# Kernel optimization log

Measured on AMD Instinct MI355X. Metric: run time of the kernel, lower is better.

Reference implementation:

```python
import jax, jax.numpy as jnp
import numpy as np

N = 100000      # nodes
E = 800000      # edges
IN1 = 128       # gcn input feature dim
IN2 = 64        # lstm input feature dim
H = 128         # hidden_channels
B = 32          # lstm batch
T = 200         # lstm seq len
OUT = 1         # out_channels
TARGET = jnp.array([0, 1000, 2000, 3000, 4000, 5000, 6000, 7000])  # numgcnE=8


def setup_inputs() -> dict:
    key = jax.random.key(0)
    ks = jax.random.split(key, 20)
    s = 0.05
    inp = {
        "data0": jax.random.normal(ks[0], (B, T, IN2), jnp.float32),
        "data1": jax.random.normal(ks[1], (N, IN1), jnp.float32),
        "edge_index": jax.random.randint(ks[2], (2, E), 0, N, dtype=jnp.int64),
        # GCNConv layers (weight stored [in, out])
        "W1": jax.random.normal(ks[3], (IN1, H), jnp.float32) * s,
        "b1": jnp.zeros((H,), jnp.float32),
        "W2": jax.random.normal(ks[4], (H, H), jnp.float32) * s,
        "b2": jnp.zeros((H,), jnp.float32),
        # LSTM1 (gate order i,f,g,o as in torch)
        "Wih1": jax.random.normal(ks[5], (4 * H, IN2), jnp.float32) * s,
        "Whh1": jax.random.normal(ks[6], (4 * H, H), jnp.float32) * s,
        "bih1": jnp.zeros((4 * H,), jnp.float32),
        "bhh1": jnp.zeros((4 * H,), jnp.float32),
        # LSTM2
        "Wih2": jax.random.normal(ks[7], (4 * H, H), jnp.float32) * s,
        "Whh2": jax.random.normal(ks[8], (4 * H, H), jnp.float32) * s,
        "bih2": jnp.zeros((4 * H,), jnp.float32),
        "bhh2": jnp.zeros((4 * H,), jnp.float32),
        # MLP head: (numgcnE+1)*H -> (numgcnE+1)*H/2 -> OUT
        "m1_w": jax.random.normal(ks[9], (9 * H, 9 * H // 2), jnp.float32) * s,
        "m1_b": jnp.zeros((9 * H // 2,), jnp.float32),
        "m2_w": jax.random.normal(ks[10], (9 * H // 2, OUT), jnp.float32) * s,
        "m2_b": jnp.zeros((OUT,), jnp.float32),
    }
    return inp


def gcn_conv(x, W, b, src, dst, n):
    # PyG GCNConv: self-loops + symmetric normalization, then scatter-add.
    xw = x @ W                                                     # [N, H]
    ones = jnp.ones(src.shape[0], xw.dtype)
    deg = jax.ops.segment_sum(ones, dst, num_segments=n) + 1.0     # +1 self-loop
    dinv = jax.lax.rsqrt(deg)                                      # [N]
    norm = dinv[src] * dinv[dst]                                   # [E]
    agg = jax.ops.segment_sum(xw[src] * norm[:, None], dst, num_segments=n)
    agg = agg + xw * (dinv * dinv)[:, None]                        # self-loop msgs
    return agg + b


def lstm_final(x_tbi, Wih, Whh, bih, bhh):
    # x_tbi: [T, Bsz, in]; returns final hidden state h_T [Bsz, H]
    Bsz = x_tbi.shape[1]
    Hh = Whh.shape[1]
    bias = bih + bhh

    def step(carry, xt):
        h, c = carry
        g = xt @ Wih.T + h @ Whh.T + bias                          # [Bsz, 4H]
        i, f, gg, o = jnp.split(g, 4, axis=-1)
        c = jax.nn.sigmoid(f) * c + jax.nn.sigmoid(i) * jnp.tanh(gg)
        h = jax.nn.sigmoid(o) * jnp.tanh(c)
        return (h, c), None

    init = (jnp.zeros((Bsz, Hh), x_tbi.dtype), jnp.zeros((Bsz, Hh), x_tbi.dtype))
    (h, c), _ = jax.lax.scan(step, init, x_tbi)
    return h


def reference(data0, data1, edge_index, W1, b1, W2, b2,
              Wih1, Whh1, bih1, bhh1, Wih2, Whh2, bih2, bhh2,
              m1_w, m1_b, m2_w, m2_b):
    src, dst = edge_index[0], edge_index[1]
    n = data1.shape[0]
    # two GCN layers with ReLU
    h = jax.nn.relu(gcn_conv(data1, W1, b1, src, dst, n))
    h = jax.nn.relu(gcn_conv(h, W2, b2, src, dst, n))
    g = h[TARGET].reshape(-1)                                      # [numgcnE*H]
    # lstm1 over [B, T, IN2] (batch_first) -> final h_n [B, H]
    h1 = lstm_final(jnp.swapaxes(data0, 0, 1), Wih1, Whh1, bih1, bhh1)
    # lstm2 consumes h_n[None] as [batch=1, seq=B, H] -> final h [1, H]
    h2 = lstm_final(h1[:, None, :], Wih2, Whh2, bih2, bhh2)[0]     # [H]
    d = jnp.concatenate([g, h2])                                   # [(numgcnE+1)*H]
    return (d @ m1_w + m1_b) @ m2_w + m2_b                         # [OUT]
```

## Files before the change

### kernel.cpp

```cpp
#include <hip/hip_runtime.h>
#include <hip/hip_bf16.h>
#include <cstring>

using bf16 = __hip_bfloat16;
typedef _Float16 h2v __attribute__((ext_vector_type(2)));
typedef _Float16 h8v __attribute__((ext_vector_type(8)));

#if __has_builtin(__builtin_amdgcn_fdot2)
__device__ __forceinline__ float FDOT2(h2v a, h2v b, float c) {
    return __builtin_amdgcn_fdot2(a, b, c, false);
}
#else
__device__ __forceinline__ float FDOT2(h2v a, h2v b, float c) {
    return c + (float)a.x * (float)b.x + (float)a.y * (float)b.y;
}
#endif

__device__ __forceinline__ float sigm_f(float x) {
    return __builtin_amdgcn_rcpf(1.f + __expf(-x));
}
__device__ __forceinline__ float tanh_f(float x) {
    return 1.f - 2.f * __builtin_amdgcn_rcpf(1.f + __expf(2.f * x));
}

__device__ __forceinline__ float xor32_get(float x) {
#if __has_builtin(__builtin_amdgcn_permlane32_swap)
    typedef unsigned uv2 __attribute__((ext_vector_type(2)));
    union { float f; unsigned u; } cv; cv.f = x;
    uv2 r = __builtin_amdgcn_permlane32_swap(cv.u, cv.u, false, false);
    union { unsigned u; float f; } rv; rv.u = r[1];
    return rv.f;
#else
    return __shfl_xor(x, 32);
#endif
}

constexpr int NH    = 128;
constexpr int G4    = 512;
constexpr int TSEQ  = 200;
constexpr int BBATCH= 32;
constexpr int NTGT  = 8;

constexpr int LCAP1 = 1024;
constexpr int S1CAP = LCAP1 + NTGT;
constexpr int LCAP2 = 8192;
constexpr int S2CAP = LCAP2 + S1CAP;

constexpr size_t algn(size_t x) { return (x + 255) & ~size_t(255); }
constexpr size_t OFF_GX1  = 0;
constexpr size_t OFF_GX2  = algn(OFF_GX1  + 6400ull * G4 * 4);
constexpr size_t OFF_DEG  = algn(OFF_GX2  + 32ull * G4 * 4);
constexpr size_t OFF_DINV = algn(OFF_DEG  + 100000ull * 4);
constexpr size_t OFF_SL1  = algn(OFF_DINV + 100000ull * 4);
constexpr size_t OFF_SL2  = algn(OFF_SL1  + 100000ull * 4);
constexpr size_t OFF_CNT  = algn(OFF_SL2  + 100000ull * 4);
constexpr size_t OFF_L1   = algn(OFF_CNT  + 64);
constexpr size_t OFF_S1   = algn(OFF_L1   + (size_t)LCAP1 * 8);
constexpr size_t OFF_L2   = algn(OFF_S1   + (size_t)S1CAP * 4);
constexpr size_t OFF_S2   = algn(OFF_L2   + (size_t)LCAP2 * 8);
constexpr size_t OFF_XW1  = algn(OFF_S2   + (size_t)S2CAP * 4);
constexpr size_t OFF_H1   = algn(OFF_XW1  + (size_t)S2CAP * NH * 4);
constexpr size_t OFF_XW2  = algn(OFF_H1   + (size_t)S1CAP * NH * 4);
constexpr size_t OFF_DVEC = algn(OFF_XW2  + (size_t)S1CAP * NH * 4);
constexpr size_t OFF_H1F  = algn(OFF_DVEC + 1152ull * 4);
constexpr size_t OFF_CACC = algn(OFF_H1F  + 32ull * NH * 4);
constexpr size_t WS_NEEDED = OFF_CACC + 576ull * 4;

__device__ __forceinline__ int edge_at(const int* ei, int E, int is64, int row, int e) {
    return is64 ? ei[(((size_t)row * E) + e) * 2] : ei[((size_t)row * E) + e];
}

__device__ __forceinline__ float dinv_of(const int* deg, int v) {
    return rsqrtf((float)deg[v] + 1.0f);
}

__global__ void k_init(const int* ei, int* deg, int* slot1, int* slot2, int* cnt,
                       float* h1, int n, unsigned int* out, unsigned int canary) {
    int i0 = blockIdx.x * 256 + threadIdx.x;
    int gstride = gridDim.x * 256;
    if (i0 < 14) cnt[i0] = 0;
    if (i0 == 15) cnt[15] = (ei[1] == 0 && ei[3] == 0 && ei[5] == 0 && ei[7] == 0) ? 1 : 0;
    if (i0 == 16) out[0] = canary;
    for (int i = i0; i < S1CAP * NH; i += gstride) h1[i] = 0.f;
    for (int i = i0; i < n; i += gstride) { deg[i] = 0; slot1[i] = -1; slot2[i] = -1; }
}

__global__ void k_deg_l1(const int* ei, int E, int* deg, int2* l1, int* cnt) {
    int is64 = cnt[15];
    for (int e = blockIdx.x * 256 + threadIdx.x; e < E; e += gridDim.x * 256) {
        int d = edge_at(ei, E, is64, 1, e);
        if ((unsigned)d < 100000u) atomicAdd(&deg[d], 1);
        if (d <= 7000 && d >= 0 && d % 1000 == 0) {
            int s = edge_at(ei, E, is64, 0, e);
            int idx = atomicAdd(&cnt[0], 1);
            if (idx < LCAP1) l1[idx] = make_int2(s, d);
        }
    }
}

__global__ void k_s1(const int2* l1, int* cnt, int* slot1, int* s1list,
                     int* slot2, int* s2list) {
    __shared__ int ns1;
    if (threadIdx.x == 0) ns1 = 0;
    __syncthreads();
    int m = min(cnt[0], LCAP1);
    for (int i = threadIdx.x; i < NTGT + m; i += blockDim.x) {
        int v = (i < NTGT) ? i * 1000 : l1[i - NTGT].x;
        if ((unsigned)v >= 100000u) continue;
        int old = atomicCAS(&slot1[v], -1, -2);
        if (old == -1) {
            int idx = atomicAdd(&ns1, 1);
            if (idx < S1CAP) { s1list[idx] = v; atomicExch(&slot1[v], idx); }
        }
    }
    __syncthreads();
    int n1 = min(ns1, S1CAP);
    if (threadIdx.x == 0) cnt[1] = n1;
    for (int i = threadIdx.x; i < n1; i += blockDim.x) {
        int v = s1list[i];
        int old = atomicCAS(&slot2[v], -1, -2);
        if (old == -1) {
            int idx = atomicAdd(&cnt[2], 1);
            if (idx < S2CAP) { s2list[idx] = v; atomicExch(&slot2[v], idx); }
        }
    }
}

__global__ void k_l2(const int* ei, int E, const int* slot1,
                     int2* l2, int* cnt, int* slot2, int* s2list) {
    int is64 = cnt[15];
    for (int e = blockIdx.x * 256 + threadIdx.x; e < E; e += gridDim.x * 256) {
        int d = edge_at(ei, E, is64, 1, e);
        if ((unsigned)d >= 100000u) continue;
        if (slot1[d] >= 0) {
            int s = edge_at(ei, E, is64, 0, e);
            if ((unsigned)s >= 100000u) continue;
            int idx = atomicAdd(&cnt[3], 1);
            if (idx < LCAP2) l2[idx] = make_int2(s, d);
            int old = atomicCAS(&slot2[s], -1, -2);
            if (old == -1) {
                int j = atomicAdd(&cnt[2], 1);
                if (j < S2CAP) { s2list[j] = s; atomicExch(&slot2[s], j); }
            }
        }
    }
}


__global__ void k_xw1(const float* x, const float* W, const int* s2list, const int* cnt, float* xw1) {
    int i = blockIdx.x;
    if (i >= min(cnt[2], S2CAP)) return;
    int node = s2list[i];
    __shared__ float xs[NH];
    int c = threadIdx.x;
    xs[c] = x[(size_t)node * NH + c];
    __syncthreads();
    float acc = 0.f;
    #pragma unroll 8
    for (int k = 0; k < NH; k++) acc += xs[k] * W[(size_t)k * NH + c];
    xw1[(size_t)i * NH + c] = acc;
}

__global__ void k_h1scat(const float* xw1, const int2* l2, const int* cnt,
                         const int* slot1, const int* slot2, const int* deg, float* h1) {
    int e = blockIdx.x;
    if (e >= min(cnt[3], LCAP2)) return;
    int2 sd = l2[e];
    int t1 = slot1[sd.y], s2 = slot2[sd.x];
    if (t1 < 0 || t1 >= S1CAP || s2 < 0 || s2 >= S2CAP) return;
    float w = dinv_of(deg, sd.x) * dinv_of(deg, sd.y);
    atomicAdd(&h1[t1 * NH + threadIdx.x],
              xw1[(size_t)s2 * NH + threadIdx.x] * w);
}

__global__ void k_xw2(const float* h1, const float* xw1, const float* W, const float* b1,
                      const int* cnt, const int* s1list, const int* slot2, const int* deg,
                      float* xw2) {
    int i = blockIdx.x;
    if (i >= min(cnt[1], S1CAP)) return;
    __shared__ float xs[NH];
    int c = threadIdx.x;
    int node = s1list[i];
    int s2i = slot2[node];
    if (s2i < 0 || s2i >= S2CAP) s2i = 0;
    float v = dinv_of(deg, node);
    xs[c] = fmaxf(h1[i * NH + c] + xw1[(size_t)s2i * NH + c] * (v * v) + b1[c], 0.f);
    __syncthreads();
    float acc = 0.f;
    #pragma unroll 8
    for (int k = 0; k < NH; k++) acc += xs[k] * W[(size_t)k * NH + c];
    xw2[(size_t)i * NH + c] = acc;
}

__global__ void k_gout(const float* xw2, const int2* l1, const int* cnt,
                       const int* slot1, const int* deg, const float* b2, float* dvec) {
    int t = blockIdx.x;
    int tgt = t * 1000;
    int c = threadIdx.x;
    float vt = dinv_of(deg, tgt);
    int st = slot1[tgt]; if (st < 0 || st >= S1CAP) st = 0;
    float acc = xw2[(size_t)st * NH + c] * vt * vt;
    int m = min(cnt[0], LCAP1);
    for (int e = 0; e < m; e++) {
        int2 sd = l1[e];
        if (sd.y == tgt) {
            int ss = slot1[sd.x];
            if (ss >= 0 && ss < S1CAP)
                acc += xw2[(size_t)ss * NH + c] * dinv_of(deg, sd.x) * vt;
        }
    }
    acc += b2[c];
    dvec[t * NH + c] = fmaxf(acc, 0.f);
}


__global__ __launch_bounds__(256) void k_gx1hw(const float* data0, const float* Wih,
                                               const float* bih, const float* bhh, float* gx,
                                               const float* m1w, const float* m1b,
                                               const float* m2w, const float* m2b, float* hw) {
    int tid = threadIdx.x;
    if (blockIdx.x >= 800) {
        int hb = blockIdx.x - 800;
        int wv = tid >> 6, ln = tid & 63;
        if (hb < 18) {
            #pragma unroll 4
            for (int rr = 0; rr < 16; rr++) {
                int row = hb * 64 + wv * 16 + rr;
                float s = 0.f;
                #pragma unroll
                for (int j = ln; j < 576; j += 64) s += m1w[(size_t)row * 576 + j] * m2w[j];
                #pragma unroll
                for (int off = 32; off > 0; off >>= 1) s += __shfl_down(s, off, 64);
                if (ln == 0) hw[row] = s;
            }
        } else if (wv == 0) {
            float s = 0.f;
            for (int j = ln; j < 576; j += 64) s += m1b[j] * m2w[j];
            #pragma unroll
            for (int off = 32; off > 0; off >>= 1) s += __shfl_down(s, off, 64);
            if (ln == 0) hw[1152] = s + m2b[0];
        }
        return;
    }
    constexpr int LDP = 68;
    __shared__ float As[64 * LDP];
    __shared__ float Bs[64 * LDP];
    int rb = blockIdx.x >> 3;
    int gb = blockIdx.x & 7;
    int r0 = rb * 64, g0 = gb * 64;
    for (int i = tid; i < 64 * 64; i += 256) {
        int rr = i >> 6, k = i & 63;
        int r = r0 + rr, b = r & 31, t = r >> 5;
        As[rr * LDP + k] = data0[((size_t)b * TSEQ + t) * 64 + k];
        Bs[rr * LDP + k] = Wih[(size_t)(g0 + rr) * 64 + k];
    }
    __syncthreads();
    int tr = (tid & 15) * 4;
    int tg = (tid >> 4) * 4;
    float acc[4][4] = {};
    #pragma unroll
    for (int k4 = 0; k4 < 16; k4++) {
        float4 a0 = *(const float4*)&As[(tr + 0) * LDP + k4 * 4];
        float4 a1 = *(const float4*)&As[(tr + 1) * LDP + k4 * 4];
        float4 a2 = *(const float4*)&As[(tr + 2) * LDP + k4 * 4];
        float4 a3 = *(const float4*)&As[(tr + 3) * LDP + k4 * 4];
        float4 b0 = *(const float4*)&Bs[(tg + 0) * LDP + k4 * 4];
        float4 b1 = *(const float4*)&Bs[(tg + 1) * LDP + k4 * 4];
        float4 b2 = *(const float4*)&Bs[(tg + 2) * LDP + k4 * 4];
        float4 b3 = *(const float4*)&Bs[(tg + 3) * LDP + k4 * 4];
        const float4 av[4] = {a0, a1, a2, a3};
        const float4 bv[4] = {b0, b1, b2, b3};
        #pragma unroll
        for (int i = 0; i < 4; i++)
            #pragma unroll
            for (int j = 0; j < 4; j++)
                acc[i][j] += av[i].x * bv[j].x + av[i].y * bv[j].y
                           + av[i].z * bv[j].z + av[i].w * bv[j].w;
    }
    float bias[4];
    #pragma unroll
    for (int j = 0; j < 4; j++) bias[j] = bih[g0 + tg + j] + bhh[g0 + tg + j];
    #pragma unroll
    for (int i = 0; i < 4; i++) {
        size_t row = (size_t)(r0 + tr + i) * G4 + g0 + tg;
        #pragma unroll
        for (int j = 0; j < 4; j++) gx[row + j] = acc[i][j] + bias[j];
    }
}

template<int T, int NB>
__global__ __launch_bounds__(256, 1) void k_lstm(const float* gx, const float* Whh, float* hfinal) {
    int b = blockIdx.x;
    int tid = threadIdx.x;
    int w = tid >> 6, l = tid & 63;
    int j = w * 32 + (l & 31);
    int role = l >> 5;
    int r0 = role ? (j + NH) : j;
    int r1 = role ? (j + 3 * NH) : (j + 2 * NH);
    __shared__ __align__(16) _Float16 hbuf[2][NH];
    h2v w0[NH / 2], w1[NH / 2];
    #pragma unroll
    for (int k = 0; k < NH; k += 4) {
        float4 a = *(const float4*)&Whh[(size_t)r0 * NH + k];
        w0[k / 2]     = h2v{(_Float16)a.x, (_Float16)a.y};
        w0[k / 2 + 1] = h2v{(_Float16)a.z, (_Float16)a.w};
        float4 c4 = *(const float4*)&Whh[(size_t)r1 * NH + k];
        w1[k / 2]     = h2v{(_Float16)c4.x, (_Float16)c4.y};
        w1[k / 2 + 1] = h2v{(_Float16)c4.z, (_Float16)c4.w};
    }
    if (tid < NH) { hbuf[0][tid] = (_Float16)0.f; hbuf[1][tid] = (_Float16)0.f; }
    float c = 0.f, hout = 0.f;
    float nx0 = gx[((size_t)0 * NB + b) * G4 + r0];
    float nx1 = gx[((size_t)0 * NB + b) * G4 + r1];
    __syncthreads();
    for (int t = 0; t < T; t++) {
        const h8v* hv8 = (const h8v*)hbuf[t & 1];
        float a0 = nx0, a1 = nx1;
        int tn = (t + 1 < T) ? (t + 1) : t;
        nx0 = gx[((size_t)tn * NB + b) * G4 + r0];
        nx1 = gx[((size_t)tn * NB + b) * G4 + r1];
        float p0 = 0.f, q0 = 0.f, p1 = 0.f, q1 = 0.f;
        #pragma unroll
        for (int m = 0; m < NH / 8; m++) {
            h8v h8 = hv8[m];
            h2v ha = __builtin_shufflevector(h8, h8, 0, 1);
            h2v hb = __builtin_shufflevector(h8, h8, 2, 3);
            h2v hc = __builtin_shufflevector(h8, h8, 4, 5);
            h2v hd = __builtin_shufflevector(h8, h8, 6, 7);
            p0 = FDOT2(w0[4 * m],     ha, p0);
            q0 = FDOT2(w0[4 * m + 1], hb, q0);
            p0 = FDOT2(w0[4 * m + 2], hc, p0);
            q0 = FDOT2(w0[4 * m + 3], hd, q0);
            p1 = FDOT2(w1[4 * m],     ha, p1);
            q1 = FDOT2(w1[4 * m + 1], hb, q1);
            p1 = FDOT2(w1[4 * m + 2], hc, p1);
            q1 = FDOT2(w1[4 * m + 3], hd, q1);
        }
        float ga = a0 + p0 + q0;
        float gb = a1 + p1 + q1;
        float s  = sigm_f(ga);
        float tg = role ? sigm_f(gb) : tanh_f(gb);
        float u  = s * tg;
        float fv = xor32_get(s);
        float ov = xor32_get(tg);
        if (role == 0) {
            c = fv * c + u;
            hout = ov * tanh_f(c);
            hbuf[(t + 1) & 1][j] = (_Float16)hout;
        }
        __syncthreads();
    }
    if (role == 0) hfinal[(size_t)b * NH + j] = hout;
}

__global__ __launch_bounds__(256, 1) void k_lstm2f(
        const float* h1f, const float* Wih, const float* bih, const float* bhh,
        const float* Whh, const float* dvec, const float* hw, unsigned int* out) {
    __shared__ float hsf[32 * NH];
    __shared__ float gxl[32 * G4];
    __shared__ __align__(16) _Float16 hbuf[2][NH];
    __shared__ float harr[NH];
    __shared__ float red[4];
    int tid = threadIdx.x;
    for (int i = tid; i < 32 * NH; i += 256) hsf[i] = h1f[i];
    if (tid < NH) { hbuf[0][tid] = (_Float16)0.f; hbuf[1][tid] = (_Float16)0.f; }
    __syncthreads();
    for (int gp = 0; gp < 2; gp++) {
        int g = tid + gp * 256;
        float wf[NH];
        #pragma unroll
        for (int k = 0; k < NH; k += 4) {
            float4 a = *(const float4*)&Wih[(size_t)g * NH + k];
            wf[k] = a.x; wf[k + 1] = a.y; wf[k + 2] = a.z; wf[k + 3] = a.w;
        }
        float bias = bih[g] + bhh[g];
        for (int t = 0; t < 32; t++) {
            const float4* hv4 = (const float4*)&hsf[t * NH];
            float p = 0.f, q = 0.f;
            #pragma unroll
            for (int m = 0; m < NH / 4; m++) {
                float4 h4 = hv4[m];
                p += wf[4 * m] * h4.x + wf[4 * m + 1] * h4.y;
                q += wf[4 * m + 2] * h4.z + wf[4 * m + 3] * h4.w;
            }
            gxl[t * G4 + g] = p + q + bias;
        }
    }
    __syncthreads();
    int w = tid >> 6, l = tid & 63;
    int j = w * 32 + (l & 31);
    int role = l >> 5;
    int r0 = role ? (j + NH) : j;
    int r1 = role ? (j + 3 * NH) : (j + 2 * NH);
    h2v w0[NH / 2], w1[NH / 2];
    #pragma unroll
    for (int k = 0; k < NH; k += 4) {
        float4 a = *(const float4*)&Whh[(size_t)r0 * NH + k];
        w0[k / 2]     = h2v{(_Float16)a.x, (_Float16)a.y};
        w0[k / 2 + 1] = h2v{(_Float16)a.z, (_Float16)a.w};
        float4 c4 = *(const float4*)&Whh[(size_t)r1 * NH + k];
        w1[k / 2]     = h2v{(_Float16)c4.x, (_Float16)c4.y};
        w1[k / 2 + 1] = h2v{(_Float16)c4.z, (_Float16)c4.w};
    }
    float c = 0.f, hout = 0.f;
    for (int t = 0; t < 32; t++) {
        const h8v* hv8 = (const h8v*)hbuf[t & 1];
        float a0 = gxl[t * G4 + r0];
        float a1 = gxl[t * G4 + r1];
        float p0 = 0.f, q0 = 0.f, p1 = 0.f, q1 = 0.f;
        #pragma unroll
        for (int m = 0; m < NH / 8; m++) {
            h8v h8 = hv8[m];
            h2v ha = __builtin_shufflevector(h8, h8, 0, 1);
            h2v hb = __builtin_shufflevector(h8, h8, 2, 3);
            h2v hc = __builtin_shufflevector(h8, h8, 4, 5);
            h2v hd = __builtin_shufflevector(h8, h8, 6, 7);
            p0 = FDOT2(w0[4 * m],     ha, p0);
            q0 = FDOT2(w0[4 * m + 1], hb, q0);
            p0 = FDOT2(w0[4 * m + 2], hc, p0);
            q0 = FDOT2(w0[4 * m + 3], hd, q0);
            p1 = FDOT2(w1[4 * m],     ha, p1);
            q1 = FDOT2(w1[4 * m + 1], hb, q1);
            p1 = FDOT2(w1[4 * m + 2], hc, p1);
            q1 = FDOT2(w1[4 * m + 3], hd, q1);
        }
        float ga = a0 + p0 + q0;
        float gb = a1 + p1 + q1;
        float s  = sigm_f(ga);
        float tg = role ? sigm_f(gb) : tanh_f(gb);
        float u  = s * tg;
        float fv = xor32_get(s);
        float ov = xor32_get(tg);
        if (role == 0) {
            c = fv * c + u;
            hout = ov * tanh_f(c);
            hbuf[(t + 1) & 1][j] = (_Float16)hout;
        }
        __syncthreads();
    }
    if (role == 0) harr[j] = hout;
    __syncthreads();
    float s = 0.f;
    for (int i = tid; i < 1024; i += 256) s += dvec[i] * hw[i];
    if (tid < NH) s += harr[tid] * hw[1024 + tid];
    #pragma unroll
    for (int off = 32; off > 0; off >>= 1) s += __shfl_down(s, off, 64);
    if ((tid & 63) == 0) red[tid >> 6] = s;
    __syncthreads();
    if (tid == 0) {
        float tot = red[0] + red[1] + red[2] + red[3] + hw[1152];
        bf16 hb = __float2bfloat16(tot);
        unsigned short u;
        memcpy(&u, &hb, 2);
        out[0] = ((unsigned int)u << 16) | u;
    }
}


extern "C" void kernel_launch(void* const* d_in, const int* in_sizes, int n_in,
                              void* d_out, int out_size, void* d_ws, size_t ws_size,
                              hipStream_t stream) {
    const float* data0 = (const float*)d_in[0];
    const float* data1 = (const float*)d_in[1];
    const int*   ei    = (const int*)d_in[2];
    const float* W1    = (const float*)d_in[3];
    const float* b1    = (const float*)d_in[4];
    const float* W2    = (const float*)d_in[5];
    const float* b2    = (const float*)d_in[6];
    const float* Wih1  = (const float*)d_in[7];
    const float* Whh1  = (const float*)d_in[8];
    const float* bih1  = (const float*)d_in[9];
    const float* bhh1  = (const float*)d_in[10];
    const float* Wih2  = (const float*)d_in[11];
    const float* Whh2  = (const float*)d_in[12];
    const float* bih2  = (const float*)d_in[13];
    const float* bhh2  = (const float*)d_in[14];
    const float* m1w   = (const float*)d_in[15];
    const float* m1b   = (const float*)d_in[16];
    const float* m2w   = (const float*)d_in[17];
    const float* m2b   = (const float*)d_in[18];

    const int n = in_sizes[1] / NH;
    const int E = in_sizes[2] / 2;

    char* ws = (char*)d_ws;
    float* gx1   = (float*)(ws + OFF_GX1);
    int*   deg   = (int*)  (ws + OFF_DEG);
    float* hw    = (float*)(ws + OFF_DINV);
    int*   slot1 = (int*)  (ws + OFF_SL1);
    int*   slot2 = (int*)  (ws + OFF_SL2);
    int*   cnt   = (int*)  (ws + OFF_CNT);
    int2*  l1    = (int2*) (ws + OFF_L1);
    int*   s1l   = (int*)  (ws + OFF_S1);
    int2*  l2    = (int2*) (ws + OFF_L2);
    int*   s2l   = (int*)  (ws + OFF_S2);
    float* xw1   = (float*)(ws + OFF_XW1);
    float* h1    = (float*)(ws + OFF_H1);
    float* xw2   = (float*)(ws + OFF_XW2);
    float* dvec  = (float*)(ws + OFF_DVEC);
    float* h1f   = (float*)(ws + OFF_H1F);

    float v = 1.0f + (ws_size < WS_NEEDED ? 1.0f : 0.0f) + (n_in != 19 ? 2.0f : 0.0f);
    unsigned int fb; memcpy(&fb, &v, 4);
    unsigned int hi = fb >> 16;
    unsigned int canary_bits = (hi << 16) | hi;

    int nb = (n + 255) / 256;
    int eb = (E + 255) / 256;

    k_init   <<<nb, 256, 0, stream>>>(ei, deg, slot1, slot2, cnt, h1, n,
                                      (unsigned int*)d_out, canary_bits);
    k_deg_l1 <<<eb, 256, 0, stream>>>(ei, E, deg, l1, cnt);
    k_s1     <<<1, 256, 0, stream>>>(l1, cnt, slot1, s1l, slot2, s2l);
    k_l2     <<<eb, 256, 0, stream>>>(ei, E, slot1, l2, cnt, slot2, s2l);
    k_xw1    <<<S2CAP, NH, 0, stream>>>(data1, W1, s2l, cnt, xw1);
    k_h1scat <<<LCAP2, NH, 0, stream>>>(xw1, l2, cnt, slot1, slot2, deg, h1);
    k_xw2    <<<S1CAP, NH, 0, stream>>>(h1, xw1, W2, b1, cnt, s1l, slot2, deg, xw2);
    k_gout   <<<NTGT, NH, 0, stream>>>(xw2, l1, cnt, slot1, deg, b2, dvec);
    k_gx1hw  <<<819, 256, 0, stream>>>(data0, Wih1, bih1, bhh1, gx1,
                                       m1w, m1b, m2w, m2b, hw);
    k_lstm<TSEQ, BBATCH><<<BBATCH, 256, 0, stream>>>(gx1, Whh1, h1f);
    k_lstm2f <<<1, 256, 0, stream>>>(h1f, Wih2, bih2, bhh2, Whh2, dvec, hw,
                                     (unsigned int*)d_out);
    (void)out_size;
}
```

Before: 480.4 us.

## Fuse LSTM2 input projection into LSTM1 kernel tail across batch blocks

After: 421.8 us. 1.14x faster.

```diff
diff --git a/kernel.cpp b/kernel.cpp
--- a/kernel.cpp
+++ b/kernel.cpp
@@ -289,7 +289,9 @@
 }
 
 template<int T, int NB>
-__global__ __launch_bounds__(256, 1) void k_lstm(const float* gx, const float* Whh, float* hfinal) {
+__global__ __launch_bounds__(256, 1) void k_lstm1g(const float* gx, const float* Whh,
+                                                   const float* Wih2, const float* bih2,
+                                                   const float* bhh2, float* gx2) {
     int b = blockIdx.x;
     int tid = threadIdx.x;
     int w = tid >> 6, l = tid & 63;
@@ -298,6 +300,7 @@
     int r0 = role ? (j + NH) : j;
     int r1 = role ? (j + 3 * NH) : (j + 2 * NH);
     __shared__ __align__(16) _Float16 hbuf[2][NH];
+    __shared__ float hfin[NH];
     h2v w0[NH / 2], w1[NH / 2];
     #pragma unroll
     for (int k = 0; k < NH; k += 4) {
@@ -350,48 +353,34 @@
         }
         __syncthreads();
     }
-    if (role == 0) hfinal[(size_t)b * NH + j] = hout;
-}
-
-__global__ __launch_bounds__(256, 1) void k_lstm2f(
-        const float* h1f, const float* Wih, const float* bih, const float* bhh,
-        const float* Whh, const float* dvec, const float* hw, unsigned int* out) {
-    __shared__ float hsf[32 * NH];
-    __shared__ float gxl[32 * G4];
-    __shared__ __align__(16) _Float16 hbuf[2][NH];
-    __shared__ float harr[NH];
-    __shared__ float red[4];
+    if (role == 0) hfin[j] = hout;
+    __syncthreads();
+    int g0 = tid, g1 = tid + 256;
+    float a0 = bih2[g0] + bhh2[g0];
+    float a1 = bih2[g1] + bhh2[g1];
+    #pragma unroll 4
+    for (int k = 0; k < NH; k++) {
+        float hk = hfin[k];
+        a0 += Wih2[(size_t)g0 * NH + k] * hk;
+        a1 += Wih2[(size_t)g1 * NH + k] * hk;
+    }
+    gx2[(size_t)b * G4 + g0] = a0;
+    gx2[(size_t)b * G4 + g1] = a1;
+}
+
+__global__ __launch_bounds__(256, 1) void k_lstm2h(const float* gx, const float* Whh,
+                                                   const float* dvec, const float* hw,
+                                                   unsigned int* out) {
+    constexpr int T = BBATCH;
     int tid = threadIdx.x;
-    for (int i = tid; i < 32 * NH; i += 256) hsf[i] = h1f[i];
-    if (tid < NH) { hbuf[0][tid] = (_Float16)0.f; hbuf[1][tid] = (_Float16)0.f; }
-    __syncthreads();
-    for (int gp = 0; gp < 2; gp++) {
-        int g = tid + gp * 256;
-        float wf[NH];
-        #pragma unroll
-        for (int k = 0; k < NH; k += 4) {
-            float4 a = *(const float4*)&Wih[(size_t)g * NH + k];
-            wf[k] = a.x; wf[k + 1] = a.y; wf[k + 2] = a.z; wf[k + 3] = a.w;
-        }
-        float bias = bih[g] + bhh[g];
-        for (int t = 0; t < 32; t++) {
-            const float4* hv4 = (const float4*)&hsf[t * NH];
-            float p = 0.f, q = 0.f;
-            #pragma unroll
-            for (int m = 0; m < NH / 4; m++) {
-                float4 h4 = hv4[m];
-                p += wf[4 * m] * h4.x + wf[4 * m + 1] * h4.y;
-                q += wf[4 * m + 2] * h4.z + wf[4 * m + 3] * h4.w;
-            }
-            gxl[t * G4 + g] = p + q + bias;
-        }
-    }
-    __syncthreads();
     int w = tid >> 6, l = tid & 63;
     int j = w * 32 + (l & 31);
     int role = l >> 5;
     int r0 = role ? (j + NH) : j;
     int r1 = role ? (j + 3 * NH) : (j + 2 * NH);
+    __shared__ __align__(16) _Float16 hbuf[2][NH];
+    __shared__ float harr[NH];
+    __shared__ float red[4];
     h2v w0[NH / 2], w1[NH / 2];
     #pragma unroll
     for (int k = 0; k < NH; k += 4) {
@@ -402,11 +391,17 @@
         w1[k / 2]     = h2v{(_Float16)c4.x, (_Float16)c4.y};
         w1[k / 2 + 1] = h2v{(_Float16)c4.z, (_Float16)c4.w};
     }
+    if (tid < NH) { hbuf[0][tid] = (_Float16)0.f; hbuf[1][tid] = (_Float16)0.f; }
     float c = 0.f, hout = 0.f;
-    for (int t = 0; t < 32; t++) {
+    float nx0 = gx[r0];
+    float nx1 = gx[r1];
+    __syncthreads();
+    for (int t = 0; t < T; t++) {
         const h8v* hv8 = (const h8v*)hbuf[t & 1];
-        float a0 = gxl[t * G4 + r0];
-        float a1 = gxl[t * G4 + r1];
+        float a0 = nx0, a1 = nx1;
+        int tn = (t + 1 < T) ? (t + 1) : t;
+        nx0 = gx[(size_t)tn * G4 + r0];
+        nx1 = gx[(size_t)tn * G4 + r1];
         float p0 = 0.f, q0 = 0.f, p1 = 0.f, q1 = 0.f;
         #pragma unroll
         for (int m = 0; m < NH / 8; m++) {
@@ -485,6 +480,7 @@
 
     char* ws = (char*)d_ws;
     float* gx1   = (float*)(ws + OFF_GX1);
+    float* gx2   = (float*)(ws + OFF_GX2);
     int*   deg   = (int*)  (ws + OFF_DEG);
     float* hw    = (float*)(ws + OFF_DINV);
     int*   slot1 = (int*)  (ws + OFF_SL1);
@@ -498,7 +494,6 @@
     float* h1    = (float*)(ws + OFF_H1);
     float* xw2   = (float*)(ws + OFF_XW2);
     float* dvec  = (float*)(ws + OFF_DVEC);
-    float* h1f   = (float*)(ws + OFF_H1F);
 
     float v = 1.0f + (ws_size < WS_NEEDED ? 1.0f : 0.0f) + (n_in != 19 ? 2.0f : 0.0f);
     unsigned int fb; memcpy(&fb, &v, 4);
@@ -519,8 +514,7 @@
     k_gout   <<<NTGT, NH, 0, stream>>>(xw2, l1, cnt, slot1, deg, b2, dvec);
     k_gx1hw  <<<819, 256, 0, stream>>>(data0, Wih1, bih1, bhh1, gx1,
                                        m1w, m1b, m2w, m2b, hw);
-    k_lstm<TSEQ, BBATCH><<<BBATCH, 256, 0, stream>>>(gx1, Whh1, h1f);
-    k_lstm2f <<<1, 256, 0, stream>>>(h1f, Wih2, bih2, bhh2, Whh2, dvec, hw,
-                                     (unsigned int*)d_out);
+    k_lstm1g<TSEQ, BBATCH><<<BBATCH, 256, 0, stream>>>(gx1, Whh1, Wih2, bih2, bhh2, gx2);
+    k_lstm2h <<<1, 256, 0, stream>>>(gx2, Whh2, dvec, hw, (unsigned int*)d_out);
     (void)out_size;
 }
```
